# Kernel optimization log

Hardware: AMD Instinct MI355X
Metric: run time of the kernel (lower is better)

## Reference

```python
import jax, jax.numpy as jnp
import numpy as np

N_NODES = 40000
N_EDGES = 640000
IN_DIM, H_DIM, OUT_DIM = 128, 128, 64


def setup_inputs() -> dict:
    key = jax.random.key(0)
    ks = jax.random.split(key, 16)
    x = jax.random.normal(ks[0], (N_NODES, IN_DIM), dtype=jnp.float32)
    edge_index = jax.random.randint(ks[1], (2, N_EDGES), 0, N_NODES, dtype=jnp.int64)
    dims = [(IN_DIM, H_DIM), (H_DIM, H_DIM), (H_DIM, OUT_DIM)]
    inp = {"x": x, "edge_index": edge_index}
    for l, (di, do) in enumerate(dims):
        s = 1.0 / np.sqrt(di)
        inp[f"Wr{l}"] = jax.random.uniform(ks[2 + 3 * l], (di, do), jnp.float32, -s, s)  # lin_rel weight
        inp[f"br{l}"] = jax.random.uniform(ks[3 + 3 * l], (do,), jnp.float32, -s, s)     # lin_rel bias
        inp[f"Ws{l}"] = jax.random.uniform(ks[4 + 3 * l], (di, do), jnp.float32, -s, s)  # lin_root weight (no bias)
    return inp


def _graph_conv(x, src, dst, Wr, br, Ws):
    # PyG GraphConv (aggr='add'): out = lin_rel(sum_{j in N(i)} x_j) + lin_root(x_i)
    agg = jax.ops.segment_sum(x[src], dst, num_segments=N_NODES)  # [N, d_in]
    return agg @ Wr + br + x @ Ws


def reference(x, edge_index, Wr0, br0, Ws0, Wr1, br1, Ws1, Wr2, br2, Ws2):
    src, dst = edge_index[0], edge_index[1]
    h = x
    for Wr, br, Ws in ((Wr0, br0, Ws0), (Wr1, br1, Ws1), (Wr2, br2, Ws2)):
        h = _graph_conv(h, src, dst, Wr, br, Ws)
        h = jax.nn.relu(h)
        # dropout p=0 / eval mode -> identity
    return jax.nn.log_softmax(h, axis=1)
```

## Files before the change

kernel.cpp:

```cpp
#include <hip/hip_runtime.h>
#include <hip/hip_bf16.h>


#define N_NODES 40000
#define N_EDGES 640000
#define PAD_NODES 40064
#define DEG_STRIDE 32
#define ROW_CAP   64

typedef float v4f __attribute__((ext_vector_type(4)));
typedef float v2f __attribute__((ext_vector_type(2)));
typedef short short8 __attribute__((ext_vector_type(8)));

__device__ inline unsigned short f2b(float f) {
    unsigned u = __float_as_uint(f);
    return (unsigned short)((u + 0x7fffu + ((u >> 16) & 1u)) >> 16);
}

__global__ __launch_bounds__(256) void prep_kernel(const float* __restrict__ Wr0, const float* __restrict__ Ws0,
                                                   const float* __restrict__ Wr1, const float* __restrict__ Ws1,
                                                   const float* __restrict__ Wr2, const float* __restrict__ Ws2,
                                                   unsigned short* __restrict__ Wt0,
                                                   unsigned short* __restrict__ Wt1,
                                                   unsigned short* __restrict__ Wt2) {
    int t = blockIdx.x * 256 + threadIdx.x;
    if (t < 32768) {
        int n = t >> 7, k = t & 127;
        const float* W = (n < 128) ? Wr0 : Ws0;
        Wt0[t] = f2b(W[k * 128 + (n & 127)]);
    } else if (t < 65536) {
        int u = t - 32768;
        int n = u >> 7, k = u & 127;
        const float* W = (n < 128) ? Wr1 : Ws1;
        Wt1[u] = f2b(W[k * 128 + (n & 127)]);
    } else if (t < 81920) {
        int u = t - 65536;
        int n = u >> 7, k = u & 127;
        const float* W = (n < 64) ? Wr2 : Ws2;
        Wt2[u] = f2b(W[k * 64 + (n & 63)]);
    }
}

__global__ __launch_bounds__(256) void place_kernel(const int* __restrict__ src,
                                                    const int* __restrict__ dst,
                                                    int* __restrict__ deg,
                                                    unsigned short* __restrict__ esrc) {
    int e = blockIdx.x * 256 + threadIdx.x;
    if (e < N_EDGES) {
        int d = dst[e];
        int r = atomicAdd(&deg[(size_t)d * DEG_STRIDE], 1);
        if (r < ROW_CAP) esrc[(size_t)d * ROW_CAP + r] = (unsigned short)src[e];
    }
}

template <int DO, bool F32>
__global__ __launch_bounds__(256, 3) void mm_kernel(const void* __restrict__ Ain,
                                                    const unsigned short* __restrict__ Wt,
                                                    unsigned short* __restrict__ T,
                                                    unsigned short* __restrict__ S) {
    __shared__ unsigned short As[128 * 64];
    __shared__ unsigned short Bs[128 * 64];

    const int tid = threadIdx.x;
    const int m0  = blockIdx.x * 128;
    const int n0  = blockIdx.y * 128;

    const int wave = tid >> 6;
    const int lane = tid & 63;
    const int wr   = (wave >> 1) * 64;
    const int wc   = (wave & 1) * 64;
    const int qm   = lane & 15;
    const int k8   = (lane >> 4) * 8;

    v4f acc[4][4];
#pragma unroll
    for (int i = 0; i < 4; i++)
#pragma unroll
        for (int j = 0; j < 4; j++) acc[i][j] = (v4f)(0.0f);

#pragma unroll
    for (int half = 0; half < 2; half++) {
        if (F32) {
            const float4* Xg = (const float4*)Ain;
#pragma unroll
            for (int i = 0; i < 8; i++) {
                int idx = i * 256 + tid;
                int row = idx >> 4, c4 = idx & 15;
                int gr = m0 + row;
                if (gr > N_NODES - 1) gr = N_NODES - 1;
                float4 v = Xg[(size_t)gr * 32 + half * 16 + c4];
                uint2 p;
                p.x = (unsigned)f2b(v.x) | ((unsigned)f2b(v.y) << 16);
                p.y = (unsigned)f2b(v.z) | ((unsigned)f2b(v.w) << 16);
                ((uint2*)As)[idx] = p;
            }
        } else {
            const unsigned short* Ab = (const unsigned short*)Ain;
#pragma unroll
            for (int i = 0; i < 4; i++) {
                int idx = i * 256 + tid;
                int row = idx >> 3, c8 = idx & 7;
                ((uint4*)As)[idx] =
                    *(const uint4*)(Ab + (size_t)(m0 + row) * 128 + half * 64 + c8 * 8);
            }
        }
        {
#pragma unroll
            for (int i = 0; i < 4; i++) {
                int idx = i * 256 + tid;
                int row = idx >> 3, c8 = idx & 7;
                ((uint4*)Bs)[idx] =
                    *(const uint4*)(Wt + (size_t)(n0 + row) * 128 + half * 64 + c8 * 8);
            }
        }
        __syncthreads();

#pragma unroll
        for (int ks = 0; ks < 2; ks++) {
            short8 af[4], bf[4];
#pragma unroll
            for (int i = 0; i < 4; i++) {
                af[i] = *(const short8*)(const void*)(As + (wr + i * 16 + qm) * 64 + ks * 32 + k8);
                bf[i] = *(const short8*)(const void*)(Bs + (wc + i * 16 + qm) * 64 + ks * 32 + k8);
            }
#pragma unroll
            for (int mi = 0; mi < 4; mi++)
#pragma unroll
                for (int ni = 0; ni < 4; ni++)
                    acc[mi][ni] = __builtin_amdgcn_mfma_f32_16x16x32_bf16(af[mi], bf[ni], acc[mi][ni], 0, 0, 0);
        }
        __syncthreads();
    }

#pragma unroll
    for (int mi = 0; mi < 4; mi++) {
        const int nodeBase = m0 + wr + mi * 16 + ((lane >> 4) << 2);
#pragma unroll
        for (int r = 0; r < 4; r++) {
            const int node = nodeBase + r;
            if (node <= N_NODES) {
                const bool real = (node < N_NODES);
#pragma unroll
                for (int ni = 0; ni < 4; ni++) {
                    const int c = wc + ni * 16 + qm;
                    const unsigned short hv = real ? f2b(acc[mi][ni][r]) : (unsigned short)0;
                    if (DO == 128) {
                        (n0 ? S : T)[(size_t)node * 128 + c] = hv;
                    } else {
                        if (c < 64) T[(size_t)node * 64 + c] = hv;
                        else        S[(size_t)node * 64 + (c - 64)] = hv;
                    }
                }
            }
        }
    }
}

__device__ inline void addp(v2f* a, uint4 q) {
    v2f t0 = { __uint_as_float(q.x << 16), __uint_as_float(q.x & 0xffff0000u) };
    v2f t1 = { __uint_as_float(q.y << 16), __uint_as_float(q.y & 0xffff0000u) };
    v2f t2 = { __uint_as_float(q.z << 16), __uint_as_float(q.z & 0xffff0000u) };
    v2f t3 = { __uint_as_float(q.w << 16), __uint_as_float(q.w & 0xffff0000u) };
    a[0] += t0; a[1] += t1; a[2] += t2; a[3] += t3;
}

template <int DO, bool LAST>
__global__ __launch_bounds__(256) void aggregate_kernel(const unsigned short* __restrict__ T,
                                                        const unsigned short* __restrict__ S,
                                                        const float* __restrict__ br,
                                                        const int* __restrict__ deg,
                                                        const unsigned short* __restrict__ esrc,
                                                        unsigned short* __restrict__ Hout,
                                                        float* __restrict__ Fout) {
    constexpr int TPN = DO / 8;
    constexpr int G   = 256 / TPN;
    const int lane = threadIdx.x % TPN;
    const int n    = blockIdx.x * G + threadIdx.x / TPN;

    int cnt = deg[(size_t)n * DEG_STRIDE];
    if (cnt > ROW_CAP) cnt = ROW_CAP;
    const unsigned short* erow = esrc + (size_t)n * ROW_CAP;
    const uint4* T4 = (const uint4*)T;

    const uint4  sv = ((const uint4*)S)[(size_t)n * TPN + lane];
    const float4 b0 = ((const float4*)br)[lane * 2];
    const float4 b1 = ((const float4*)br)[lane * 2 + 1];

    v2f acc[4];
    acc[0] = (v2f)(0.0f); acc[1] = (v2f)(0.0f);
    acc[2] = (v2f)(0.0f); acc[3] = (v2f)(0.0f);

    for (int o = 0; o < cnt; o += 8) {
        uint4 iv = *(const uint4*)(erow + o);
        unsigned j0 = iv.x & 0xffffu, j1 = iv.x >> 16;
        unsigned j2 = iv.y & 0xffffu, j3 = iv.y >> 16;
        unsigned j4 = iv.z & 0xffffu, j5 = iv.z >> 16;
        unsigned j6 = iv.w & 0xffffu, j7 = iv.w >> 16;
        j0 = (o + 0 < cnt) ? j0 : N_NODES;
        j1 = (o + 1 < cnt) ? j1 : N_NODES;
        j2 = (o + 2 < cnt) ? j2 : N_NODES;
        j3 = (o + 3 < cnt) ? j3 : N_NODES;
        j4 = (o + 4 < cnt) ? j4 : N_NODES;
        j5 = (o + 5 < cnt) ? j5 : N_NODES;
        j6 = (o + 6 < cnt) ? j6 : N_NODES;
        j7 = (o + 7 < cnt) ? j7 : N_NODES;
        uint4 q0 = T4[(size_t)j0 * TPN + lane];
        uint4 q1 = T4[(size_t)j1 * TPN + lane];
        uint4 q2 = T4[(size_t)j2 * TPN + lane];
        uint4 q3 = T4[(size_t)j3 * TPN + lane];
        uint4 q4 = T4[(size_t)j4 * TPN + lane];
        uint4 q5 = T4[(size_t)j5 * TPN + lane];
        uint4 q6 = T4[(size_t)j6 * TPN + lane];
        uint4 q7 = T4[(size_t)j7 * TPN + lane];
        addp(acc, q0); addp(acc, q1); addp(acc, q2); addp(acc, q3);
        addp(acc, q4); addp(acc, q5); addp(acc, q6); addp(acc, q7);
    }
    addp(acc, sv);

    float v[8];
    v[0] = fmaxf(acc[0].x + b0.x, 0.f); v[1] = fmaxf(acc[0].y + b0.y, 0.f);
    v[2] = fmaxf(acc[1].x + b0.z, 0.f); v[3] = fmaxf(acc[1].y + b0.w, 0.f);
    v[4] = fmaxf(acc[2].x + b1.x, 0.f); v[5] = fmaxf(acc[2].y + b1.y, 0.f);
    v[6] = fmaxf(acc[3].x + b1.z, 0.f); v[7] = fmaxf(acc[3].y + b1.w, 0.f);

    if (LAST) {
        float m = v[0];
#pragma unroll
        for (int i = 1; i < 8; i++) m = fmaxf(m, v[i]);
#pragma unroll
        for (int off = 4; off; off >>= 1) m = fmaxf(m, __shfl_xor(m, off, 64));
        float es = 0.f;
#pragma unroll
        for (int i = 0; i < 8; i++) es += expf(v[i] - m);
#pragma unroll
        for (int off = 4; off; off >>= 1) es += __shfl_xor(es, off, 64);
        float lse = m + logf(es);
        float4 o0 = make_float4(v[0] - lse, v[1] - lse, v[2] - lse, v[3] - lse);
        float4 o1 = make_float4(v[4] - lse, v[5] - lse, v[6] - lse, v[7] - lse);
        ((float4*)Fout)[(size_t)n * 16 + lane * 2]     = o0;
        ((float4*)Fout)[(size_t)n * 16 + lane * 2 + 1] = o1;
    } else {
        uint4 o;
        o.x = (unsigned)f2b(v[0]) | ((unsigned)f2b(v[1]) << 16);
        o.y = (unsigned)f2b(v[2]) | ((unsigned)f2b(v[3]) << 16);
        o.z = (unsigned)f2b(v[4]) | ((unsigned)f2b(v[5]) << 16);
        o.w = (unsigned)f2b(v[6]) | ((unsigned)f2b(v[7]) << 16);
        ((uint4*)Hout)[(size_t)n * TPN + lane] = o;
    }
}


extern "C" void kernel_launch(void* const* d_in, const int* in_sizes, int n_in,
                              void* d_out, int out_size, void* d_ws, size_t ws_size,
                              hipStream_t stream) {
    const float* x    = (const float*)d_in[0];
    const int*   eidx = (const int*)d_in[1];
    const float* Wr0  = (const float*)d_in[2];
    const float* br0  = (const float*)d_in[3];
    const float* Ws0  = (const float*)d_in[4];
    const float* Wr1  = (const float*)d_in[5];
    const float* br1  = (const float*)d_in[6];
    const float* Ws1  = (const float*)d_in[7];
    const float* Wr2  = (const float*)d_in[8];
    const float* br2  = (const float*)d_in[9];
    const float* Ws2  = (const float*)d_in[10];
    float* out = (float*)d_out;

    const int* src = eidx;
    const int* dst = eidx + N_EDGES;

    auto align = [](size_t v) { return (v + 255) & ~(size_t)255; };
    char* w = (char*)d_ws;
    int* deg  = (int*)w;             w += align(sizeof(int) * (size_t)N_NODES * DEG_STRIDE);
    unsigned short* esrc = (unsigned short*)w;
    w += align(sizeof(unsigned short) * (size_t)N_NODES * ROW_CAP);
    unsigned short* H1b = (unsigned short*)w;  w += align(2ull * PAD_NODES * 128);
    unsigned short* H2b = (unsigned short*)w;  w += align(2ull * PAD_NODES * 128);
    unsigned short* Wt0 = (unsigned short*)w;  w += align(2ull * 256 * 128);
    unsigned short* Wt1 = (unsigned short*)w;  w += align(2ull * 256 * 128);
    unsigned short* Wt2 = (unsigned short*)w;  w += align(2ull * 128 * 128);
    unsigned short* T   = (unsigned short*)w;  w += align(2ull * PAD_NODES * 128);
    unsigned short* Sb  = (unsigned short*)w;  w += align(2ull * PAD_NODES * 128);
    (void)ws_size; (void)n_in; (void)in_sizes; (void)out_size;

    hipMemsetAsync(deg, 0, sizeof(int) * (size_t)N_NODES * DEG_STRIDE, stream);
    prep_kernel<<<320, 256, 0, stream>>>(Wr0, Ws0, Wr1, Ws1, Wr2, Ws2, Wt0, Wt1, Wt2);

    place_kernel<<<(N_EDGES + 255) / 256, 256, 0, stream>>>(src, dst, deg, esrc);

    mm_kernel<128, true><<<dim3(PAD_NODES / 128, 2), 256, 0, stream>>>(x, Wt0, T, Sb);
    aggregate_kernel<128, false><<<N_NODES / 16, 256, 0, stream>>>(T, Sb, br0, deg, esrc, H1b, nullptr);

    mm_kernel<128, false><<<dim3(PAD_NODES / 128, 2), 256, 0, stream>>>(H1b, Wt1, T, Sb);
    aggregate_kernel<128, false><<<N_NODES / 16, 256, 0, stream>>>(T, Sb, br1, deg, esrc, H2b, nullptr);

    mm_kernel<64, false><<<dim3(PAD_NODES / 128, 1), 256, 0, stream>>>(H2b, Wt2, T, Sb);
    aggregate_kernel<64, true><<<N_NODES / 32, 256, 0, stream>>>(T, Sb, br2, deg, esrc, nullptr, out);
}
```

Before: 216.2 us.

## Split gathered features into column planes and compact degree array

The mm kernel now writes the gathered T matrix as four 32-column planes, each 64 bytes per node. The 128-wide aggregation is split into per-plane blocks, interleaved so neighbouring blocks share a plane. Each plane is about 2.5 MB, so random neighbour gathers should hit a smaller, cache-resident working set. The degree array is also compacted from a 32-int stride to a dense array, and its zeroing is folded into the prep kernel in place of a separate memset. The trade-off is four times as many aggregation blocks, each re-reading the edge lists and degrees, and atomics on the now-adjacent degree counters may contend more.

```diff
diff --git a/kernel.cpp b/kernel.cpp
--- a/kernel.cpp
+++ b/kernel.cpp
@@ -5,8 +5,9 @@
 #define N_NODES 40000
 #define N_EDGES 640000
 #define PAD_NODES 40064
-#define DEG_STRIDE 32
+#define DEG_CAP   40960
 #define ROW_CAP   64
+#define QPLANE    (40064 * 32)
 
 typedef float v4f __attribute__((ext_vector_type(4)));
 typedef float v2f __attribute__((ext_vector_type(2)));
@@ -22,22 +23,28 @@
                                                    const float* __restrict__ Wr2, const float* __restrict__ Ws2,
                                                    unsigned short* __restrict__ Wt0,
                                                    unsigned short* __restrict__ Wt1,
-                                                   unsigned short* __restrict__ Wt2) {
-    int t = blockIdx.x * 256 + threadIdx.x;
-    if (t < 32768) {
-        int n = t >> 7, k = t & 127;
-        const float* W = (n < 128) ? Wr0 : Ws0;
-        Wt0[t] = f2b(W[k * 128 + (n & 127)]);
-    } else if (t < 65536) {
-        int u = t - 32768;
-        int n = u >> 7, k = u & 127;
-        const float* W = (n < 128) ? Wr1 : Ws1;
-        Wt1[u] = f2b(W[k * 128 + (n & 127)]);
-    } else if (t < 81920) {
-        int u = t - 65536;
-        int n = u >> 7, k = u & 127;
-        const float* W = (n < 64) ? Wr2 : Ws2;
-        Wt2[u] = f2b(W[k * 64 + (n & 63)]);
+                                                   unsigned short* __restrict__ Wt2,
+                                                   int* __restrict__ deg) {
+    int tid = blockIdx.x * 256 + threadIdx.x;
+    if (tid < DEG_CAP / 4) {
+        ((int4*)deg)[tid] = make_int4(0, 0, 0, 0);
+    } else {
+        int t = tid - DEG_CAP / 4;
+        if (t < 32768) {
+            int n = t >> 7, k = t & 127;
+            const float* W = (n < 128) ? Wr0 : Ws0;
+            Wt0[t] = f2b(W[k * 128 + (n & 127)]);
+        } else if (t < 65536) {
+            int u = t - 32768;
+            int n = u >> 7, k = u & 127;
+            const float* W = (n < 128) ? Wr1 : Ws1;
+            Wt1[u] = f2b(W[k * 128 + (n & 127)]);
+        } else if (t < 81920) {
+            int u = t - 65536;
+            int n = u >> 7, k = u & 127;
+            const float* W = (n < 64) ? Wr2 : Ws2;
+            Wt2[u] = f2b(W[k * 64 + (n & 63)]);
+        }
     }
 }
 
@@ -48,7 +55,7 @@
     int e = blockIdx.x * 256 + threadIdx.x;
     if (e < N_EDGES) {
         int d = dst[e];
-        int r = atomicAdd(&deg[(size_t)d * DEG_STRIDE], 1);
+        int r = atomicAdd(&deg[d], 1);
         if (r < ROW_CAP) esrc[(size_t)d * ROW_CAP + r] = (unsigned short)src[e];
     }
 }
@@ -145,7 +152,8 @@
                     const int c = wc + ni * 16 + qm;
                     const unsigned short hv = real ? f2b(acc[mi][ni][r]) : (unsigned short)0;
                     if (DO == 128) {
-                        (n0 ? S : T)[(size_t)node * 128 + c] = hv;
+                        if (n0) S[(size_t)node * 128 + c] = hv;
+                        else    T[(size_t)(c >> 5) * QPLANE + (size_t)node * 32 + (c & 31)] = hv;
                     } else {
                         if (c < 64) T[(size_t)node * 64 + c] = hv;
                         else        S[(size_t)node * 64 + (c - 64)] = hv;
@@ -164,20 +172,84 @@
     a[0] += t0; a[1] += t1; a[2] += t2; a[3] += t3;
 }
 
-template <int DO, bool LAST>
-__global__ __launch_bounds__(256) void aggregate_kernel(const unsigned short* __restrict__ T,
-                                                        const unsigned short* __restrict__ S,
-                                                        const float* __restrict__ br,
-                                                        const int* __restrict__ deg,
-                                                        const unsigned short* __restrict__ esrc,
-                                                        unsigned short* __restrict__ Hout,
-                                                        float* __restrict__ Fout) {
-    constexpr int TPN = DO / 8;
-    constexpr int G   = 256 / TPN;
+__global__ __launch_bounds__(256) void aggregate_q_kernel(const unsigned short* __restrict__ T,
+                                                          const unsigned short* __restrict__ S,
+                                                          const float* __restrict__ br,
+                                                          const int* __restrict__ deg,
+                                                          const unsigned short* __restrict__ esrc,
+                                                          unsigned short* __restrict__ Hout) {
+    const int bid = blockIdx.x;
+    const int q   = (bid & 7) >> 1;
+    const int s   = (bid >> 3) * 2 + (bid & 1);
+    if (s >= N_NODES / 64) return;
+    const int lane4 = threadIdx.x & 3;
+    const int n     = s * 64 + (threadIdx.x >> 2);
+
+    int cnt = deg[n];
+    if (cnt > ROW_CAP) cnt = ROW_CAP;
+    const unsigned short* erow = esrc + (size_t)n * ROW_CAP;
+    const uint4* T4 = (const uint4*)(T + (size_t)q * QPLANE);
+
+    const uint4  sv = ((const uint4*)S)[(size_t)n * 16 + q * 4 + lane4];
+    const float4 b0 = ((const float4*)br)[q * 8 + lane4 * 2];
+    const float4 b1 = ((const float4*)br)[q * 8 + lane4 * 2 + 1];
+
+    v2f acc[4];
+    acc[0] = (v2f)(0.0f); acc[1] = (v2f)(0.0f);
+    acc[2] = (v2f)(0.0f); acc[3] = (v2f)(0.0f);
+
+    for (int o = 0; o < cnt; o += 8) {
+        uint4 iv = *(const uint4*)(erow + o);
+        unsigned j0 = iv.x & 0xffffu, j1 = iv.x >> 16;
+        unsigned j2 = iv.y & 0xffffu, j3 = iv.y >> 16;
+        unsigned j4 = iv.z & 0xffffu, j5 = iv.z >> 16;
+        unsigned j6 = iv.w & 0xffffu, j7 = iv.w >> 16;
+        j0 = (o + 0 < cnt) ? j0 : N_NODES;
+        j1 = (o + 1 < cnt) ? j1 : N_NODES;
+        j2 = (o + 2 < cnt) ? j2 : N_NODES;
+        j3 = (o + 3 < cnt) ? j3 : N_NODES;
+        j4 = (o + 4 < cnt) ? j4 : N_NODES;
+        j5 = (o + 5 < cnt) ? j5 : N_NODES;
+        j6 = (o + 6 < cnt) ? j6 : N_NODES;
+        j7 = (o + 7 < cnt) ? j7 : N_NODES;
+        uint4 q0 = T4[(size_t)j0 * 4 + lane4];
+        uint4 q1 = T4[(size_t)j1 * 4 + lane4];
+        uint4 q2 = T4[(size_t)j2 * 4 + lane4];
+        uint4 q3 = T4[(size_t)j3 * 4 + lane4];
+        uint4 q4 = T4[(size_t)j4 * 4 + lane4];
+        uint4 q5 = T4[(size_t)j5 * 4 + lane4];
+        uint4 q6 = T4[(size_t)j6 * 4 + lane4];
+        uint4 q7 = T4[(size_t)j7 * 4 + lane4];
+        addp(acc, q0); addp(acc, q1); addp(acc, q2); addp(acc, q3);
+        addp(acc, q4); addp(acc, q5); addp(acc, q6); addp(acc, q7);
+    }
+    addp(acc, sv);
+
+    float v[8];
+    v[0] = fmaxf(acc[0].x + b0.x, 0.f); v[1] = fmaxf(acc[0].y + b0.y, 0.f);
+    v[2] = fmaxf(acc[1].x + b0.z, 0.f); v[3] = fmaxf(acc[1].y + b0.w, 0.f);
+    v[4] = fmaxf(acc[2].x + b1.x, 0.f); v[5] = fmaxf(acc[2].y + b1.y, 0.f);
+    v[6] = fmaxf(acc[3].x + b1.z, 0.f); v[7] = fmaxf(acc[3].y + b1.w, 0.f);
+
+    uint4 o;
+    o.x = (unsigned)f2b(v[0]) | ((unsigned)f2b(v[1]) << 16);
+    o.y = (unsigned)f2b(v[2]) | ((unsigned)f2b(v[3]) << 16);
+    o.z = (unsigned)f2b(v[4]) | ((unsigned)f2b(v[5]) << 16);
+    o.w = (unsigned)f2b(v[6]) | ((unsigned)f2b(v[7]) << 16);
+    ((uint4*)Hout)[(size_t)n * 16 + q * 4 + lane4] = o;
+}
+
+__global__ __launch_bounds__(256) void aggregate_last_kernel(const unsigned short* __restrict__ T,
+                                                             const unsigned short* __restrict__ S,
+                                                             const float* __restrict__ br,
+                                                             const int* __restrict__ deg,
+                                                             const unsigned short* __restrict__ esrc,
+                                                             float* __restrict__ Fout) {
+    constexpr int TPN = 8;
     const int lane = threadIdx.x % TPN;
-    const int n    = blockIdx.x * G + threadIdx.x / TPN;
-
-    int cnt = deg[(size_t)n * DEG_STRIDE];
+    const int n    = blockIdx.x * 32 + threadIdx.x / TPN;
+
+    int cnt = deg[n];
     if (cnt > ROW_CAP) cnt = ROW_CAP;
     const unsigned short* erow = esrc + (size_t)n * ROW_CAP;
     const uint4* T4 = (const uint4*)T;
@@ -223,30 +295,21 @@
     v[4] = fmaxf(acc[2].x + b1.x, 0.f); v[5] = fmaxf(acc[2].y + b1.y, 0.f);
     v[6] = fmaxf(acc[3].x + b1.z, 0.f); v[7] = fmaxf(acc[3].y + b1.w, 0.f);
 
-    if (LAST) {
-        float m = v[0];
-#pragma unroll
-        for (int i = 1; i < 8; i++) m = fmaxf(m, v[i]);
-#pragma unroll
-        for (int off = 4; off; off >>= 1) m = fmaxf(m, __shfl_xor(m, off, 64));
-        float es = 0.f;
-#pragma unroll
-        for (int i = 0; i < 8; i++) es += expf(v[i] - m);
-#pragma unroll
-        for (int off = 4; off; off >>= 1) es += __shfl_xor(es, off, 64);
-        float lse = m + logf(es);
-        float4 o0 = make_float4(v[0] - lse, v[1] - lse, v[2] - lse, v[3] - lse);
-        float4 o1 = make_float4(v[4] - lse, v[5] - lse, v[6] - lse, v[7] - lse);
-        ((float4*)Fout)[(size_t)n * 16 + lane * 2]     = o0;
-        ((float4*)Fout)[(size_t)n * 16 + lane * 2 + 1] = o1;
-    } else {
-        uint4 o;
-        o.x = (unsigned)f2b(v[0]) | ((unsigned)f2b(v[1]) << 16);
-        o.y = (unsigned)f2b(v[2]) | ((unsigned)f2b(v[3]) << 16);
-        o.z = (unsigned)f2b(v[4]) | ((unsigned)f2b(v[5]) << 16);
-        o.w = (unsigned)f2b(v[6]) | ((unsigned)f2b(v[7]) << 16);
-        ((uint4*)Hout)[(size_t)n * TPN + lane] = o;
-    }
+    float m = v[0];
+#pragma unroll
+    for (int i = 1; i < 8; i++) m = fmaxf(m, v[i]);
+#pragma unroll
+    for (int off = 4; off; off >>= 1) m = fmaxf(m, __shfl_xor(m, off, 64));
+    float es = 0.f;
+#pragma unroll
+    for (int i = 0; i < 8; i++) es += expf(v[i] - m);
+#pragma unroll
+    for (int off = 4; off; off >>= 1) es += __shfl_xor(es, off, 64);
+    float lse = m + logf(es);
+    float4 o0 = make_float4(v[0] - lse, v[1] - lse, v[2] - lse, v[3] - lse);
+    float4 o1 = make_float4(v[4] - lse, v[5] - lse, v[6] - lse, v[7] - lse);
+    ((float4*)Fout)[(size_t)n * 16 + lane * 2]     = o0;
+    ((float4*)Fout)[(size_t)n * 16 + lane * 2 + 1] = o1;
 }
 
 
@@ -271,7 +334,7 @@
 
     auto align = [](size_t v) { return (v + 255) & ~(size_t)255; };
     char* w = (char*)d_ws;
-    int* deg  = (int*)w;             w += align(sizeof(int) * (size_t)N_NODES * DEG_STRIDE);
+    int* deg  = (int*)w;             w += align(sizeof(int) * DEG_CAP);
     unsigned short* esrc = (unsigned short*)w;
     w += align(sizeof(unsigned short) * (size_t)N_NODES * ROW_CAP);
     unsigned short* H1b = (unsigned short*)w;  w += align(2ull * PAD_NODES * 128);
@@ -283,17 +346,17 @@
     unsigned short* Sb  = (unsigned short*)w;  w += align(2ull * PAD_NODES * 128);
     (void)ws_size; (void)n_in; (void)in_sizes; (void)out_size;
 
-    hipMemsetAsync(deg, 0, sizeof(int) * (size_t)N_NODES * DEG_STRIDE, stream);
-    prep_kernel<<<320, 256, 0, stream>>>(Wr0, Ws0, Wr1, Ws1, Wr2, Ws2, Wt0, Wt1, Wt2);
+    prep_kernel<<<(DEG_CAP / 4 + 81920 + 255) / 256, 256, 0, stream>>>(
+        Wr0, Ws0, Wr1, Ws1, Wr2, Ws2, Wt0, Wt1, Wt2, deg);
 
     place_kernel<<<(N_EDGES + 255) / 256, 256, 0, stream>>>(src, dst, deg, esrc);
 
     mm_kernel<128, true><<<dim3(PAD_NODES / 128, 2), 256, 0, stream>>>(x, Wt0, T, Sb);
-    aggregate_kernel<128, false><<<N_NODES / 16, 256, 0, stream>>>(T, Sb, br0, deg, esrc, H1b, nullptr);
+    aggregate_q_kernel<<<2504, 256, 0, stream>>>(T, Sb, br0, deg, esrc, H1b);
 
     mm_kernel<128, false><<<dim3(PAD_NODES / 128, 2), 256, 0, stream>>>(H1b, Wt1, T, Sb);
-    aggregate_kernel<128, false><<<N_NODES / 16, 256, 0, stream>>>(T, Sb, br1, deg, esrc, H2b, nullptr);
+    aggregate_q_kernel<<<2504, 256, 0, stream>>>(T, Sb, br1, deg, esrc, H2b);
 
     mm_kernel<64, false><<<dim3(PAD_NODES / 128, 1), 256, 0, stream>>>(H2b, Wt2, T, Sb);
-    aggregate_kernel<64, true><<<N_NODES / 32, 256, 0, stream>>>(T, Sb, br2, deg, esrc, nullptr, out);
-}
+    aggregate_last_kernel<<<N_NODES / 32, 256, 0, stream>>>(T, Sb, br2, deg, esrc, out);
+}
```

Measured after the change: 216.8 us. About the same (+0.3%).
